# Kernel tuning notes

Measured on AMD Instinct MI355X. Metric: run time of the kernel, lower is better.

## Reference

```python
import jax, jax.numpy as jnp
import numpy as np

C = 4          # num_components
B = 2          # true batch
HEADS = 24
DIM_HEAD = 64
D = HEADS * DIM_HEAD      # 1536, attn.out_dim == query dim
CROSS = 2048              # encoder hidden dim
S = 2048                  # latent sequence length
E = 77                    # encoder sequence length
PAD = 77                  # pad_length (must equal E for the broadcast in the original code)


def setup_inputs() -> dict:
    key = jax.random.key(0)
    ks = jax.random.split(key, 12)
    w = 0.02
    return {
        "hidden_states": jax.random.normal(ks[0], (B * C, S, D), jnp.float32),
        "encoder_hidden_states": jax.random.normal(ks[1], (B * C, E, CROSS), jnp.float32),
        "Wq": jax.random.normal(ks[2], (D, D), jnp.float32) * w,
        "bq": jax.random.normal(ks[3], (D,), jnp.float32) * w,
        "Wk": jax.random.normal(ks[4], (D, CROSS), jnp.float32) * w,
        "bk": jax.random.normal(ks[5], (D,), jnp.float32) * w,
        "Wv": jax.random.normal(ks[6], (D, CROSS), jnp.float32) * w,
        "bv": jax.random.normal(ks[7], (D,), jnp.float32) * w,
        "Wo": jax.random.normal(ks[8], (D, D), jnp.float32) * w,
        "bo": jax.random.normal(ks[9], (D,), jnp.float32) * w,
        "pad_length": PAD,
    }


def reference(hidden_states, encoder_hidden_states, Wq, bq, Wk, bk, Wv, bv, Wo, bo, pad_length):
    BC, S_, D_ = hidden_states.shape
    E_ = encoder_hidden_states.shape[1]
    Bsz = BC // C
    scale = 1.0 / np.sqrt(DIM_HEAD)

    # projections (torch nn.Linear: x @ W.T + b)
    q = hidden_states @ Wq.T + bq                      # [BC, S, D]
    k = encoder_hidden_states @ Wk.T + bk              # [BC, E, D]
    v = encoder_hidden_states @ Wv.T + bv              # [BC, E, D]
    # pad branch: to_k/to_v applied to zeros -> just the bias, broadcast over pad tokens
    k_pad = jnp.broadcast_to(bk, (BC, pad_length, D_))  # [BC, PAD, D]
    v_pad = jnp.broadcast_to(bv, (BC, pad_length, D_))
    v = jnp.concatenate([v, v_pad], axis=1)            # [BC, E+PAD, D]

    # split heads
    qh = q.reshape(BC, S_, HEADS, DIM_HEAD)
    kh = k.reshape(BC, E_, HEADS, DIM_HEAD)
    kph = k_pad.reshape(BC, pad_length, HEADS, DIM_HEAD)
    vh = v.reshape(BC, E_ + pad_length, HEADS, DIM_HEAD)

    # scores: [BC, H, S, E] and [BC, H, S, PAD]
    scores = jnp.einsum("bihd,bjhd->bhij", qh, kh) * scale
    scores_pad = jnp.einsum("bihd,bjhd->bhij", qh, kph) * scale

    # component-wise softmax: view as [C, B, H, S, *], softmax over component axis 0
    scores = scores.reshape(C, Bsz, HEADS, S_, E_)
    scores_pad = scores_pad.reshape(C, Bsz, HEADS, S_, pad_length)
    w_main = jax.nn.softmax(scores, axis=0)
    w_pad = jax.nn.softmax(scores_pad, axis=0) * (C / pad_length) * (1.0 - w_main)

    w_main = w_main.reshape(BC, HEADS, S_, E_)
    w_pad = w_pad.reshape(BC, HEADS, S_, pad_length)
    weights = jnp.concatenate([w_main, w_pad], axis=-1)  # [BC, H, S, E+PAD]

    # attention @ V -> merge heads
    out = jnp.einsum("bhij,bjhd->bihd", weights, vh).reshape(BC, S_, D_)
    out = out @ Wo.T + bo   # to_out[0]; dropout is identity in eval
    return out
```

## Files before the change

kernel.cpp:

```cpp
#include <hip/hip_runtime.h>
#include <hip/hip_bf16.h>


typedef __attribute__((ext_vector_type(8))) short short8;
typedef __attribute__((ext_vector_type(4))) float f32x4;
typedef __attribute__((ext_vector_type(4))) _Float16 half4;

#define DEV __device__ __forceinline__

DEV ushort f2bf(float x) {
  __hip_bfloat16 h = __float2bfloat16(x);
  return *reinterpret_cast<ushort*>(&h);
}


__global__ __launch_bounds__(256) void cvt_f32_bf16(const float* __restrict__ in,
                                                    ushort* __restrict__ out, int n4) {
  int idx = blockIdx.x * blockDim.x + threadIdx.x;
  int stride = gridDim.x * blockDim.x;
  for (int q = idx; q < n4; q += stride) {
    float4 f = reinterpret_cast<const float4*>(in)[q];
    ushort4 o;
    o.x = f2bf(f.x); o.y = f2bf(f.y); o.z = f2bf(f.z); o.w = f2bf(f.w);
    reinterpret_cast<ushort4*>(out)[q] = o;
  }
}

__global__ __launch_bounds__(256) void cvt_w4(const float* __restrict__ w0, ushort* __restrict__ o0, int m0,
                                              const float* __restrict__ w1, ushort* __restrict__ o1, int m1,
                                              const float* __restrict__ w2, ushort* __restrict__ o2, int m2,
                                              const float* __restrict__ w3, ushort* __restrict__ o3, int m3) {
  const float* in; ushort* out; int n4;
  switch (blockIdx.y) {
    case 0: in = w0; out = o0; n4 = m0; break;
    case 1: in = w1; out = o1; n4 = m1; break;
    case 2: in = w2; out = o2; n4 = m2; break;
    default: in = w3; out = o3; n4 = m3; break;
  }
  int idx = blockIdx.x * blockDim.x + threadIdx.x;
  int stride = gridDim.x * blockDim.x;
  for (int q = idx; q < n4; q += stride) {
    float4 f = reinterpret_cast<const float4*>(in)[q];
    ushort4 o;
    o.x = f2bf(f.x); o.y = f2bf(f.y); o.z = f2bf(f.z); o.w = f2bf(f.w);
    reinterpret_cast<ushort4*>(out)[q] = o;
  }
}

__global__ __launch_bounds__(256) void cvt_pad_ehs(const float* __restrict__ in,
                                                   ushort* __restrict__ out) {
  int q = blockIdx.x * blockDim.x + threadIdx.x;
  if (q >= 640 * 2048 / 4) return;
  int r = (q * 4) >> 11;
  ushort4 o;
  if (r < 616) {
    float4 f = reinterpret_cast<const float4*>(in)[q];
    o.x = f2bf(f.x); o.y = f2bf(f.y); o.z = f2bf(f.z); o.w = f2bf(f.w);
  } else {
    o.x = 0; o.y = 0; o.z = 0; o.w = 0;
  }
  reinterpret_cast<ushort4*>(out)[q] = o;
}


template <typename OutT>
DEV void gemm_body(const ushort* __restrict__ A, const ushort* __restrict__ B,
                   const float* __restrict__ bias, OutT* __restrict__ C,
                   int M, int N, int K) {
  __shared__ __align__(16) ushort lds[32768];
  const int tid = threadIdx.x;
  const int lane = tid & 63;
  const int wid = tid >> 6;
  const int wr = wid >> 1, wc = wid & 1;
  const long m0 = (long)blockIdx.x * 128;
  const long n0 = (long)blockIdx.y * 128;
  const int ll = lane & 15, g = lane >> 4;
  const int swz = ll & 7;

  const int srow = wid * 8 + (lane >> 3);
  const int scol = ((lane & 7) ^ (lane >> 3)) * 8;
  const ushort* pa = A + (m0 + srow) * (long)K + scol;
  const ushort* pb = B + (n0 + srow) * (long)K + scol;
  const long qstep = 32 * (long)K;

  f32x4 acc[4][4] = {};

#define STAGE(tt, bsel)                                                                    \
  do {                                                                                     \
    const long kt_ = (long)(tt) * 64;                                                      \
    const int ab_ = (bsel) * 32768 + wid * 1024;                                           \
    _Pragma("unroll") for (int q = 0; q < 4; ++q)                                          \
        __builtin_amdgcn_global_load_lds(                                                  \
            (const __attribute__((address_space(1))) void*)(pa + kt_ + q * qstep),         \
            (__attribute__((address_space(3))) void*)((char*)lds + ab_ + q * 4096),        \
            16, 0, 0);                                                                     \
    _Pragma("unroll") for (int q = 0; q < 4; ++q)                                          \
        __builtin_amdgcn_global_load_lds(                                                  \
            (const __attribute__((address_space(1))) void*)(pb + kt_ + q * qstep),         \
            (__attribute__((address_space(3))) void*)((char*)lds + ab_ + 16384 + q * 4096),\
            16, 0, 0);                                                                     \
  } while (0)

  const int nt = K >> 6;
  STAGE(0, 0);
  STAGE(1, 1);
  asm volatile("s_waitcnt vmcnt(8)" ::: "memory");
  __builtin_amdgcn_s_barrier();

  for (int t = 0; t < nt; ++t) {
    const int buf = t & 1;
    const char* abase = (const char*)lds + buf * 32768;
    const char* bbase = abase + 16384;
    short8 af[4][2], bfr[4][2];
#pragma unroll
    for (int m = 0; m < 4; ++m)
#pragma unroll
      for (int ks = 0; ks < 2; ++ks)
        af[m][ks] = *reinterpret_cast<const short8*>(
            abase + (wr * 64 + m * 16 + ll) * 128 + (((ks * 4 + g) ^ swz) * 16));
#pragma unroll
    for (int n = 0; n < 4; ++n)
#pragma unroll
      for (int ks = 0; ks < 2; ++ks)
        bfr[n][ks] = *reinterpret_cast<const short8*>(
            bbase + (wc * 64 + n * 16 + ll) * 128 + (((ks * 4 + g) ^ swz) * 16));
    asm volatile("s_waitcnt lgkmcnt(0)" ::: "memory");
    __builtin_amdgcn_s_barrier();

    if (t < nt - 2) {
      STAGE(t + 2, buf);
      asm volatile("s_waitcnt vmcnt(8)" ::: "memory");
    } else if (t == nt - 2) {
      asm volatile("s_waitcnt vmcnt(0)" ::: "memory");
    }
    __builtin_amdgcn_sched_barrier(0);
    __builtin_amdgcn_s_setprio(1);
#pragma unroll
    for (int ks = 0; ks < 2; ++ks)
#pragma unroll
      for (int m = 0; m < 4; ++m)
#pragma unroll
        for (int n = 0; n < 4; ++n)
          acc[m][n] =
              __builtin_amdgcn_mfma_f32_16x16x32_bf16(af[m][ks], bfr[n][ks], acc[m][n], 0, 0, 0);
    __builtin_amdgcn_s_setprio(0);
    __builtin_amdgcn_s_barrier();
  }
#undef STAGE

#pragma unroll
  for (int m = 0; m < 4; ++m) {
#pragma unroll
    for (int n = 0; n < 4; ++n) {
      const int row = wr * 64 + m * 16 + g * 4;
      const int col = wc * 64 + n * 16 + ll;
      const float bias_v = bias[n0 + col];
#pragma unroll
      for (int r = 0; r < 4; ++r) {
        float val = acc[m][n][r] + bias_v;
        long off = (m0 + row + r) * (long)N + n0 + col;
        if constexpr (sizeof(OutT) == 2) {
          C[off] = (OutT)f2bf(val);
        } else {
          C[off] = val;
        }
      }
    }
  }
}

template <typename OutT>
__global__ __launch_bounds__(256) void gemm_p(const ushort* __restrict__ A,
                                              const ushort* __restrict__ B,
                                              const float* __restrict__ bias,
                                              OutT* __restrict__ C, int M, int N, int K) {
  gemm_body<OutT>(A, B, bias, C, M, N, K);
}

__global__ __launch_bounds__(256) void gemm_p_kv(const ushort* __restrict__ A,
                                                 const ushort* __restrict__ Bk,
                                                 const float* __restrict__ bk, float* Ck,
                                                 const ushort* __restrict__ Bv,
                                                 const float* __restrict__ bv, float* Cv,
                                                 int M, int N, int K) {
  if (blockIdx.z == 0)
    gemm_body<float>(A, Bk, bk, Ck, M, N, K);
  else
    gemm_body<float>(A, Bv, bv, Cv, M, N, K);
}


__global__ __launch_bounds__(256) void prep_kv(const float* __restrict__ k_f,
                                               const float* __restrict__ v_f,
                                               const float* __restrict__ bk,
                                               const float* __restrict__ bv,
                                               ushort* __restrict__ kimg,
                                               ushort* __restrict__ vimg) {
  __shared__ _Float16 vl[80][68];
  const int c = blockIdx.x, h = blockIdx.y, bb = blockIdx.z;
  const int tid = threadIdx.x;
  const long ibase = ((long)(bb * 24 + h)) * 20480 + c * 5120;

  for (int rr = tid; rr < 640; rr += 256) {
    int j = rr >> 3, t = rr & 7;
    short8 v = {};
    const float* src = nullptr;
    if (j < 77)
      src = k_f + ((long)((c * 2 + bb) * 77 + j)) * 1536 + h * 64 + t * 8;
    else if (j == 77)
      src = bk + h * 64 + t * 8;
    if (src) {
      float4 f0 = reinterpret_cast<const float4*>(src)[0];
      float4 f1 = reinterpret_cast<const float4*>(src)[1];
      v[0] = f2bf(f0.x); v[1] = f2bf(f0.y); v[2] = f2bf(f0.z); v[3] = f2bf(f0.w);
      v[4] = f2bf(f1.x); v[5] = f2bf(f1.y); v[6] = f2bf(f1.z); v[7] = f2bf(f1.w);
    }
    *reinterpret_cast<short8*>(kimg + ibase + j * 64 + (t ^ (j & 7)) * 8) = v;
  }
  for (int rr = tid; rr < 640; rr += 256) {
    int j = rr >> 3, t = rr & 7;
    half4 lo = {}, hi = {};
    const float* src = nullptr;
    if (j < 77)
      src = v_f + ((long)((c * 2 + bb) * 77 + j)) * 1536 + h * 64 + t * 8;
    else if (j == 77)
      src = bv + h * 64 + t * 8;
    if (src) {
      float4 f0 = reinterpret_cast<const float4*>(src)[0];
      float4 f1 = reinterpret_cast<const float4*>(src)[1];
      lo[0] = (_Float16)f0.x; lo[1] = (_Float16)f0.y; lo[2] = (_Float16)f0.z; lo[3] = (_Float16)f0.w;
      hi[0] = (_Float16)f1.x; hi[1] = (_Float16)f1.y; hi[2] = (_Float16)f1.z; hi[3] = (_Float16)f1.w;
    }
    *reinterpret_cast<half4*>(&vl[j][t * 8]) = lo;
    *reinterpret_cast<half4*>(&vl[j][t * 8 + 4]) = hi;
  }
  __syncthreads();
  const int d = tid & 63, jg = tid >> 6;
  ushort* vrow = vimg + ibase + d * 80;
  const int x = (d >> 2) & 3;
#pragma unroll
  for (int b = 0; b < 5; ++b) {
    int jb = jg * 5 + b;
    half4 hv;
#pragma unroll
    for (int e = 0; e < 4; ++e) hv[e] = vl[jb * 4 + e][d];
    *reinterpret_cast<half4*>(vrow + ((jb ^ x) << 2)) = hv;
  }
}


__global__ __launch_bounds__(256) void attn_v3(const ushort* __restrict__ qg,
                                               const ushort* __restrict__ kimg,
                                               const ushort* __restrict__ vimg,
                                               ushort* __restrict__ ao) {
  __shared__ __align__(16) ushort kl[20480];
  __shared__ __align__(16) ushort vt[20480];
  const int tid = threadIdx.x;
  const int lane = tid & 63;
  const int w = tid >> 6;
  const int h = blockIdx.y, bb = blockIdx.z;
  const int i0 = blockIdx.x * 64;
  const long ib = ((long)(bb * 24 + h)) * 20480;

#pragma unroll
  for (int p = 0; p < 10; ++p) {
    int is = p * 4 + w;
    __builtin_amdgcn_global_load_lds(
        (const __attribute__((address_space(1))) void*)(kimg + ib + is * 512 + lane * 8),
        (__attribute__((address_space(3))) void*)((char*)kl + is * 1024), 16, 0, 0);
    __builtin_amdgcn_global_load_lds(
        (const __attribute__((address_space(1))) void*)(vimg + ib + is * 512 + lane * 8),
        (__attribute__((address_space(3))) void*)((char*)vt + is * 1024), 16, 0, 0);
  }
  __syncthreads();

  const int ll = lane & 15, g = lane >> 4;

  f32x4 s[4][5];
#pragma unroll
  for (int c = 0; c < 4; ++c)
#pragma unroll
    for (int m = 0; m < 5; ++m) s[c][m] = (f32x4){0.f, 0.f, 0.f, 0.f};

#pragma unroll
  for (int c = 0; c < 4; ++c) {
    const ushort* qbase =
        qg + ((long)((c * 2 + bb) * 2048 + i0 + w * 16 + ll)) * 1536 + h * 64 + g * 8;
    short8 qf0 = *reinterpret_cast<const short8*>(qbase);
    short8 qf1 = *reinterpret_cast<const short8*>(qbase + 32);
#pragma unroll
    for (int m = 0; m < 5; ++m) {
      const char* base = (const char*)kl + c * 10240 + (m * 16 + ll) * 128;
      short8 a0 = *reinterpret_cast<const short8*>(base + ((g ^ (ll & 7)) * 16));
      short8 a1 = *reinterpret_cast<const short8*>(base + (((4 + g) ^ (ll & 7)) * 16));
      s[c][m] = __builtin_amdgcn_mfma_f32_16x16x32_bf16(a0, qf0, s[c][m], 0, 0, 0);
      s[c][m] = __builtin_amdgcn_mfma_f32_16x16x32_bf16(a1, qf1, s[c][m], 0, 0, 0);
    }
  }

  const float scale = 0.125f;
  float wsum0 = 0.f, wsum1 = 0.f, wsum2 = 0.f, wsum3 = 0.f;
#pragma unroll
  for (int m = 0; m < 5; ++m) {
#pragma unroll
    for (int e = 0; e < 4; ++e) {
      float x0 = s[0][m][e] * scale, x1 = s[1][m][e] * scale;
      float x2 = s[2][m][e] * scale, x3 = s[3][m][e] * scale;
      float mx = fmaxf(fmaxf(x0, x1), fmaxf(x2, x3));
      float e0 = __expf(x0 - mx), e1 = __expf(x1 - mx);
      float e2 = __expf(x2 - mx), e3 = __expf(x3 - mx);
      float inv = __fdividef(1.f, e0 + e1 + e2 + e3);
      float w0 = e0 * inv, w1 = e1 * inv, w2 = e2 * inv, w3 = e3 * inv;
      int jj = m * 16 + g * 4 + e;
      float msk = (jj < 77) ? 1.f : 0.f;
      wsum0 += w0 * msk; wsum1 += w1 * msk; wsum2 += w2 * msk; wsum3 += w3 * msk;
      s[0][m][e] = w0; s[1][m][e] = w1; s[2][m][e] = w2; s[3][m][e] = w3;
    }
  }
  wsum0 += __shfl_xor(wsum0, 16); wsum0 += __shfl_xor(wsum0, 32);
  wsum1 += __shfl_xor(wsum1, 16); wsum1 += __shfl_xor(wsum1, 32);
  wsum2 += __shfl_xor(wsum2, 16); wsum2 += __shfl_xor(wsum2, 32);
  wsum3 += __shfl_xor(wsum3, 16); wsum3 += __shfl_xor(wsum3, 32);

  const bool g3 = (g == 3);
  {
    float wsum[4] = {wsum0, wsum1, wsum2, wsum3};
#pragma unroll
    for (int c = 0; c < 4; ++c) {
      float w77 = s[c][4][1];
      float pwv = w77 * (4.0f / 77.0f) * (77.0f - wsum[c]);
      s[c][4][1] = g3 ? pwv : w77;
      s[c][4][2] = g3 ? 0.f : s[c][4][2];
      s[c][4][3] = g3 ? 0.f : s[c][4][3];
    }
  }

  half4 wf[4][5];
#pragma unroll
  for (int c = 0; c < 4; ++c)
#pragma unroll
    for (int m = 0; m < 5; ++m) {
      half4 hv;
      hv[0] = (_Float16)s[c][m][0];
      hv[1] = (_Float16)s[c][m][1];
      hv[2] = (_Float16)s[c][m][2];
      hv[3] = (_Float16)s[c][m][3];
      wf[c][m] = hv;
    }

  f32x4 o[4][4];
#pragma unroll
  for (int c = 0; c < 4; ++c)
#pragma unroll
    for (int n = 0; n < 4; ++n) o[c][n] = (f32x4){0.f, 0.f, 0.f, 0.f};

#pragma unroll
  for (int c = 0; c < 4; ++c)
#pragma unroll
    for (int m = 0; m < 5; ++m)
#pragma unroll
      for (int n = 0; n < 4; ++n) {
        const int dd = n * 16 + ll;
        const int jb = (m * 4 + g) ^ ((dd >> 2) & 3);
        half4 vf = *reinterpret_cast<const half4*>(
            reinterpret_cast<const _Float16*>(vt) + c * 5120 + dd * 80 + (jb << 2));
        o[c][n] = __builtin_amdgcn_mfma_f32_16x16x16f16(wf[c][m], vf, o[c][n], 0, 0, 0);
      }

#pragma unroll
  for (int c = 0; c < 4; ++c)
#pragma unroll
    for (int n = 0; n < 4; ++n)
#pragma unroll
      for (int r = 0; r < 4; ++r) {
        long row = (long)((c * 2 + bb) * 2048 + i0 + w * 16 + g * 4 + r);
        ao[row * 1536 + h * 64 + n * 16 + ll] = f2bf(o[c][n][r]);
      }
}


extern "C" void kernel_launch(void* const* d_in, const int* in_sizes, int n_in,
                              void* d_out, int out_size, void* d_ws, size_t ws_size,
                              hipStream_t stream) {
  (void)in_sizes; (void)n_in; (void)out_size; (void)ws_size;
  const float* hs  = (const float*)d_in[0];
  const float* ehs = (const float*)d_in[1];
  const float* Wq  = (const float*)d_in[2];
  const float* bq  = (const float*)d_in[3];
  const float* Wk  = (const float*)d_in[4];
  const float* bk  = (const float*)d_in[5];
  const float* Wv  = (const float*)d_in[6];
  const float* bv  = (const float*)d_in[7];
  const float* Wo  = (const float*)d_in[8];
  const float* bo  = (const float*)d_in[9];
  float* out = (float*)d_out;

  char* ws = (char*)d_ws;
  size_t off = 0;
  auto alloc = [&](size_t bytes) {
    char* p = ws + off;
    off += (bytes + 255) & ~(size_t)255;
    return p;
  };
  ushort* hs_bf  = (ushort*)alloc(16384UL * 1536 * 2);
  ushort* ehs_bf = (ushort*)alloc(640UL * 2048 * 2);
  ushort* Wq_bf  = (ushort*)alloc(1536UL * 1536 * 2);
  ushort* Wk_bf  = (ushort*)alloc(1536UL * 2048 * 2);
  ushort* Wv_bf  = (ushort*)alloc(1536UL * 2048 * 2);
  ushort* Wo_bf  = (ushort*)alloc(1536UL * 1536 * 2);
  ushort* q_bf   = (ushort*)alloc(16384UL * 1536 * 2);
  float*  k_f    = (float*)alloc(640UL * 1536 * 4);
  float*  v_f    = (float*)alloc(640UL * 1536 * 4);
  ushort* ao_bf  = (ushort*)alloc(16384UL * 1536 * 2);
  ushort* kimg   = (ushort*)alloc(48UL * 20480 * 2);
  ushort* vimg   = (ushort*)alloc(48UL * 20480 * 2);

  dim3 b256(256);
  cvt_f32_bf16<<<2048, b256, 0, stream>>>(hs, hs_bf, 16384 * 1536 / 4);
  cvt_pad_ehs<<<(640 * 2048 / 4 + 255) / 256, b256, 0, stream>>>(ehs, ehs_bf);
  cvt_w4<<<dim3(768, 4), b256, 0, stream>>>(Wq, Wq_bf, 1536 * 1536 / 4,
                                            Wk, Wk_bf, 1536 * 2048 / 4,
                                            Wv, Wv_bf, 1536 * 2048 / 4,
                                            Wo, Wo_bf, 1536 * 1536 / 4);

  gemm_p_kv<<<dim3(5, 12, 2), b256, 0, stream>>>(ehs_bf, Wk_bf, bk, k_f, Wv_bf, bv, v_f,
                                                 640, 1536, 2048);
  prep_kv<<<dim3(4, 24, 2), b256, 0, stream>>>(k_f, v_f, bk, bv, kimg, vimg);
  gemm_p<ushort><<<dim3(128, 12), b256, 0, stream>>>(hs_bf, Wq_bf, bq, q_bf, 16384, 1536, 1536);
  attn_v3<<<dim3(32, 24, 2), b256, 0, stream>>>(q_bf, kimg, vimg, ao_bf);
  gemm_p<float><<<dim3(128, 12), b256, 0, stream>>>(ao_bf, Wo_bf, bo, out, 16384, 1536, 1536);
}
```

Before: 270.4 us.

## Replace Q/O projection GEMMs with 256x256-tile double-buffered direct-to-LDS kernel

Adds a new GEMM kernel with 256x256 output tiles, 512 threads, 128KB of dynamic LDS double-buffered through global_load_lds, XCD-aware block swizzling and split MFMA phases with priority hints. It is used for the large Q and output projections in place of the 128x128 kernel, to raise data reuse per tile and overlap loads with compute. It also merges the three fp32-to-bf16 conversion launches into a single kernel. The large LDS footprint and register pressure limit occupancy, and the 384-block grid may leave some CUs with an uneven share of work.

```diff
diff --git a/kernel.cpp b/kernel.cpp
--- a/kernel.cpp
+++ b/kernel.cpp
@@ -14,52 +14,43 @@
 }
 
 
-__global__ __launch_bounds__(256) void cvt_f32_bf16(const float* __restrict__ in,
-                                                    ushort* __restrict__ out, int n4) {
+__global__ __launch_bounds__(256) void cvt_all(const float* __restrict__ hs, ushort* __restrict__ hs_bf,
+                                               const float* __restrict__ Wq, ushort* __restrict__ Wq_bf,
+                                               const float* __restrict__ Wk, ushort* __restrict__ Wk_bf,
+                                               const float* __restrict__ Wv, ushort* __restrict__ Wv_bf,
+                                               const float* __restrict__ Wo, ushort* __restrict__ Wo_bf,
+                                               const float* __restrict__ ehs, ushort* __restrict__ ehs_bf) {
+  const int b0 = 6291456;
+  const int b1 = b0 + 589824;
+  const int b2 = b1 + 786432;
+  const int b3 = b2 + 786432;
+  const int b4 = b3 + 589824;
+  const int total = b4 + 327680;
   int idx = blockIdx.x * blockDim.x + threadIdx.x;
   int stride = gridDim.x * blockDim.x;
-  for (int q = idx; q < n4; q += stride) {
-    float4 f = reinterpret_cast<const float4*>(in)[q];
+  for (int q = idx; q < total; q += stride) {
+    const float* in; ushort* out; int qq;
+    bool zero = false;
+    if (q < b0)      { in = hs;  out = hs_bf;  qq = q; }
+    else if (q < b1) { in = Wq;  out = Wq_bf;  qq = q - b0; }
+    else if (q < b2) { in = Wk;  out = Wk_bf;  qq = q - b1; }
+    else if (q < b3) { in = Wv;  out = Wv_bf;  qq = q - b2; }
+    else if (q < b4) { in = Wo;  out = Wo_bf;  qq = q - b3; }
+    else {
+      qq = q - b4;
+      int r = qq >> 9;
+      in = ehs; out = ehs_bf;
+      zero = (r >= 616);
+    }
     ushort4 o;
-    o.x = f2bf(f.x); o.y = f2bf(f.y); o.z = f2bf(f.z); o.w = f2bf(f.w);
-    reinterpret_cast<ushort4*>(out)[q] = o;
-  }
-}
-
-__global__ __launch_bounds__(256) void cvt_w4(const float* __restrict__ w0, ushort* __restrict__ o0, int m0,
-                                              const float* __restrict__ w1, ushort* __restrict__ o1, int m1,
-                                              const float* __restrict__ w2, ushort* __restrict__ o2, int m2,
-                                              const float* __restrict__ w3, ushort* __restrict__ o3, int m3) {
-  const float* in; ushort* out; int n4;
-  switch (blockIdx.y) {
-    case 0: in = w0; out = o0; n4 = m0; break;
-    case 1: in = w1; out = o1; n4 = m1; break;
-    case 2: in = w2; out = o2; n4 = m2; break;
-    default: in = w3; out = o3; n4 = m3; break;
-  }
-  int idx = blockIdx.x * blockDim.x + threadIdx.x;
-  int stride = gridDim.x * blockDim.x;
-  for (int q = idx; q < n4; q += stride) {
-    float4 f = reinterpret_cast<const float4*>(in)[q];
-    ushort4 o;
-    o.x = f2bf(f.x); o.y = f2bf(f.y); o.z = f2bf(f.z); o.w = f2bf(f.w);
-    reinterpret_cast<ushort4*>(out)[q] = o;
-  }
-}
-
-__global__ __launch_bounds__(256) void cvt_pad_ehs(const float* __restrict__ in,
-                                                   ushort* __restrict__ out) {
-  int q = blockIdx.x * blockDim.x + threadIdx.x;
-  if (q >= 640 * 2048 / 4) return;
-  int r = (q * 4) >> 11;
-  ushort4 o;
-  if (r < 616) {
-    float4 f = reinterpret_cast<const float4*>(in)[q];
-    o.x = f2bf(f.x); o.y = f2bf(f.y); o.z = f2bf(f.z); o.w = f2bf(f.w);
-  } else {
-    o.x = 0; o.y = 0; o.z = 0; o.w = 0;
-  }
-  reinterpret_cast<ushort4*>(out)[q] = o;
+    if (!zero) {
+      float4 f = reinterpret_cast<const float4*>(in)[qq];
+      o.x = f2bf(f.x); o.y = f2bf(f.y); o.z = f2bf(f.z); o.w = f2bf(f.w);
+    } else {
+      o.x = 0; o.y = 0; o.z = 0; o.w = 0;
+    }
+    reinterpret_cast<ushort4*>(out)[qq] = o;
+  }
 }
 
 
@@ -169,14 +160,6 @@
   }
 }
 
-template <typename OutT>
-__global__ __launch_bounds__(256) void gemm_p(const ushort* __restrict__ A,
-                                              const ushort* __restrict__ B,
-                                              const float* __restrict__ bias,
-                                              OutT* __restrict__ C, int M, int N, int K) {
-  gemm_body<OutT>(A, B, bias, C, M, N, K);
-}
-
 __global__ __launch_bounds__(256) void gemm_p_kv(const ushort* __restrict__ A,
                                                  const ushort* __restrict__ Bk,
                                                  const float* __restrict__ bk, float* Ck,
@@ -187,6 +170,139 @@
     gemm_body<float>(A, Bk, bk, Ck, M, N, K);
   else
     gemm_body<float>(A, Bv, bv, Cv, M, N, K);
+}
+
+
+template <typename OutT>
+__global__ __launch_bounds__(512, 2) void gemm256(const ushort* __restrict__ A,
+                                                  const ushort* __restrict__ B,
+                                                  const float* __restrict__ bias,
+                                                  OutT* __restrict__ C,
+                                                  int M, int N, int K, int nnx) {
+  extern __shared__ char dynlds[];
+  const int tid = threadIdx.x;
+  const int lane = tid & 63;
+  const int w = tid >> 6;
+  const int wr = w >> 2, wc = w & 3;
+  const int ll = lane & 15, g = lane >> 4;
+  const int swz = ll & 7;
+
+  const int cpx = gridDim.x >> 3;
+  const int sw = (blockIdx.x & 7) * cpx + (blockIdx.x >> 3);
+  const long m0 = (long)(sw / nnx) * 256;
+  const long n0 = (long)(sw % nnx) * 256;
+
+  const int srow = tid >> 3;
+  const int scol = ((tid & 7) ^ ((tid >> 3) & 7)) * 8;
+  const ushort* pa = A + (m0 + srow) * (long)K + scol;
+  const ushort* pb = B + (n0 + srow) * (long)K + scol;
+  const long rstep = 64 * (long)K;
+
+  f32x4 acc[8][4] = {};
+
+#define STAGE2(tt, bsel)                                                                    \
+  do {                                                                                      \
+    const long kt_ = (long)(tt) * 64;                                                       \
+    char* ab_ = dynlds + (bsel) * 65536;                                                    \
+    _Pragma("unroll") for (int q = 0; q < 4; ++q)                                           \
+        __builtin_amdgcn_global_load_lds(                                                   \
+            (const __attribute__((address_space(1))) void*)(pa + kt_ + q * rstep),          \
+            (__attribute__((address_space(3))) void*)(ab_ + q * 8192 + tid * 16),           \
+            16, 0, 0);                                                                      \
+    _Pragma("unroll") for (int q = 0; q < 4; ++q)                                           \
+        __builtin_amdgcn_global_load_lds(                                                   \
+            (const __attribute__((address_space(1))) void*)(pb + kt_ + q * rstep),          \
+            (__attribute__((address_space(3))) void*)(ab_ + 32768 + q * 8192 + tid * 16),   \
+            16, 0, 0);                                                                      \
+  } while (0)
+
+  const int nt = K >> 6;
+  STAGE2(0, 0);
+  STAGE2(1, 1);
+  asm volatile("s_waitcnt vmcnt(8)" ::: "memory");
+  __builtin_amdgcn_s_barrier();
+  __builtin_amdgcn_sched_barrier(0);
+
+  for (int t = 0; t < nt; ++t) {
+    const int buf = t & 1;
+    const char* abase = dynlds + buf * 65536;
+    const char* bbase = abase + 32768;
+    short8 alo[4][2], bfr[4][2], ahi[4][2];
+#pragma unroll
+    for (int m = 0; m < 4; ++m)
+#pragma unroll
+      for (int ks = 0; ks < 2; ++ks)
+        alo[m][ks] = *reinterpret_cast<const short8*>(
+            abase + (wr * 128 + m * 16 + ll) * 128 + (((ks * 4 + g) ^ swz) * 16));
+#pragma unroll
+    for (int n = 0; n < 4; ++n)
+#pragma unroll
+      for (int ks = 0; ks < 2; ++ks)
+        bfr[n][ks] = *reinterpret_cast<const short8*>(
+            bbase + (wc * 64 + n * 16 + ll) * 128 + (((ks * 4 + g) ^ swz) * 16));
+    asm volatile("s_waitcnt lgkmcnt(0)" ::: "memory");
+    __builtin_amdgcn_sched_barrier(0);
+    __builtin_amdgcn_s_setprio(1);
+#pragma unroll
+    for (int ks = 0; ks < 2; ++ks)
+#pragma unroll
+      for (int m = 0; m < 4; ++m)
+#pragma unroll
+        for (int n = 0; n < 4; ++n)
+          acc[m][n] =
+              __builtin_amdgcn_mfma_f32_16x16x32_bf16(alo[m][ks], bfr[n][ks], acc[m][n], 0, 0, 0);
+    __builtin_amdgcn_s_setprio(0);
+#pragma unroll
+    for (int m = 0; m < 4; ++m)
+#pragma unroll
+      for (int ks = 0; ks < 2; ++ks)
+        ahi[m][ks] = *reinterpret_cast<const short8*>(
+            abase + (wr * 128 + 64 + m * 16 + ll) * 128 + (((ks * 4 + g) ^ swz) * 16));
+    asm volatile("s_waitcnt lgkmcnt(0)" ::: "memory");
+    __builtin_amdgcn_sched_barrier(0);
+    __builtin_amdgcn_s_barrier();
+
+    if (t < nt - 2) {
+      STAGE2(t + 2, buf);
+      asm volatile("s_waitcnt vmcnt(8)" ::: "memory");
+    } else if (t == nt - 2) {
+      asm volatile("s_waitcnt vmcnt(0)" ::: "memory");
+    }
+    __builtin_amdgcn_sched_barrier(0);
+    __builtin_amdgcn_s_setprio(1);
+#pragma unroll
+    for (int ks = 0; ks < 2; ++ks)
+#pragma unroll
+      for (int m = 0; m < 4; ++m)
+#pragma unroll
+        for (int n = 0; n < 4; ++n)
+          acc[4 + m][n] =
+              __builtin_amdgcn_mfma_f32_16x16x32_bf16(ahi[m][ks], bfr[n][ks], acc[4 + m][n], 0, 0, 0);
+    __builtin_amdgcn_s_setprio(0);
+    __builtin_amdgcn_s_barrier();
+    __builtin_amdgcn_sched_barrier(0);
+  }
+#undef STAGE2
+
+#pragma unroll
+  for (int m = 0; m < 8; ++m) {
+#pragma unroll
+    for (int n = 0; n < 4; ++n) {
+      const int row = wr * 128 + m * 16 + g * 4;
+      const int col = wc * 64 + n * 16 + ll;
+      const float bias_v = bias[n0 + col];
+#pragma unroll
+      for (int r = 0; r < 4; ++r) {
+        float val = acc[m][n][r] + bias_v;
+        long off = (m0 + row + r) * (long)N + n0 + col;
+        if constexpr (sizeof(OutT) == 2) {
+          C[off] = (OutT)f2bf(val);
+        } else {
+          C[off] = val;
+        }
+      }
+    }
+  }
 }
 
 
@@ -415,18 +531,19 @@
   ushort* kimg   = (ushort*)alloc(48UL * 20480 * 2);
   ushort* vimg   = (ushort*)alloc(48UL * 20480 * 2);
 
+  hipFuncSetAttribute(reinterpret_cast<const void*>(&gemm256<ushort>),
+                      hipFuncAttributeMaxDynamicSharedMemorySize, 131072);
+  hipFuncSetAttribute(reinterpret_cast<const void*>(&gemm256<float>),
+                      hipFuncAttributeMaxDynamicSharedMemorySize, 131072);
+
   dim3 b256(256);
-  cvt_f32_bf16<<<2048, b256, 0, stream>>>(hs, hs_bf, 16384 * 1536 / 4);
-  cvt_pad_ehs<<<(640 * 2048 / 4 + 255) / 256, b256, 0, stream>>>(ehs, ehs_bf);
-  cvt_w4<<<dim3(768, 4), b256, 0, stream>>>(Wq, Wq_bf, 1536 * 1536 / 4,
-                                            Wk, Wk_bf, 1536 * 2048 / 4,
-                                            Wv, Wv_bf, 1536 * 2048 / 4,
-                                            Wo, Wo_bf, 1536 * 1536 / 4);
+  cvt_all<<<4096, b256, 0, stream>>>(hs, hs_bf, Wq, Wq_bf, Wk, Wk_bf, Wv, Wv_bf,
+                                     Wo, Wo_bf, ehs, ehs_bf);
 
   gemm_p_kv<<<dim3(5, 12, 2), b256, 0, stream>>>(ehs_bf, Wk_bf, bk, k_f, Wv_bf, bv, v_f,
                                                  640, 1536, 2048);
   prep_kv<<<dim3(4, 24, 2), b256, 0, stream>>>(k_f, v_f, bk, bv, kimg, vimg);
-  gemm_p<ushort><<<dim3(128, 12), b256, 0, stream>>>(hs_bf, Wq_bf, bq, q_bf, 16384, 1536, 1536);
+  gemm256<ushort><<<384, 512, 131072, stream>>>(hs_bf, Wq_bf, bq, q_bf, 16384, 1536, 1536, 6);
   attn_v3<<<dim3(32, 24, 2), b256, 0, stream>>>(q_bf, kimg, vimg, ao_bf);
-  gemm_p<float><<<dim3(128, 12), b256, 0, stream>>>(ao_bf, Wo_bf, bo, out, 16384, 1536, 1536);
-}
+  gemm256<float><<<384, 512, 131072, stream>>>(ao_bf, Wo_bf, bo, out, 16384, 1536, 1536, 6);
+}
```

After: 288.4 us. 6.7% more time.

## Merge conversion kernels and read K fragments directly from global memory

Applied to the files above, without the earlier changes.

Folds the three f32-to-bf16 conversion kernels into a single grid-stride kernel, removing two launches. In the attention kernel, K is no longer staged in LDS: each wave loads its MFMA K fragments straight from the pre-swizzled global image. The V LDS load is issued up front and its barrier moved after the softmax, so the V copy overlaps the QK and softmax work. This halves LDS use per block, which may raise occupancy, at the cost of redundant global or L2 reads of K across the four waves.

```diff
diff --git a/kernel.cpp b/kernel.cpp
--- a/kernel.cpp
+++ b/kernel.cpp
@@ -14,52 +14,43 @@
 }
 
 
-__global__ __launch_bounds__(256) void cvt_f32_bf16(const float* __restrict__ in,
-                                                    ushort* __restrict__ out, int n4) {
+__global__ __launch_bounds__(256) void cvt_all(const float* __restrict__ hs, ushort* __restrict__ hs_bf,
+                                               const float* __restrict__ Wq, ushort* __restrict__ Wq_bf,
+                                               const float* __restrict__ Wk, ushort* __restrict__ Wk_bf,
+                                               const float* __restrict__ Wv, ushort* __restrict__ Wv_bf,
+                                               const float* __restrict__ Wo, ushort* __restrict__ Wo_bf,
+                                               const float* __restrict__ ehs, ushort* __restrict__ ehs_bf) {
+  const int b0 = 6291456;
+  const int b1 = b0 + 589824;
+  const int b2 = b1 + 786432;
+  const int b3 = b2 + 786432;
+  const int b4 = b3 + 589824;
+  const int total = b4 + 327680;
   int idx = blockIdx.x * blockDim.x + threadIdx.x;
   int stride = gridDim.x * blockDim.x;
-  for (int q = idx; q < n4; q += stride) {
-    float4 f = reinterpret_cast<const float4*>(in)[q];
+  for (int q = idx; q < total; q += stride) {
+    const float* in; ushort* out; int qq;
+    bool zero = false;
+    if (q < b0)      { in = hs;  out = hs_bf;  qq = q; }
+    else if (q < b1) { in = Wq;  out = Wq_bf;  qq = q - b0; }
+    else if (q < b2) { in = Wk;  out = Wk_bf;  qq = q - b1; }
+    else if (q < b3) { in = Wv;  out = Wv_bf;  qq = q - b2; }
+    else if (q < b4) { in = Wo;  out = Wo_bf;  qq = q - b3; }
+    else {
+      qq = q - b4;
+      int r = qq >> 9;
+      in = ehs; out = ehs_bf;
+      zero = (r >= 616);
+    }
     ushort4 o;
-    o.x = f2bf(f.x); o.y = f2bf(f.y); o.z = f2bf(f.z); o.w = f2bf(f.w);
-    reinterpret_cast<ushort4*>(out)[q] = o;
-  }
-}
-
-__global__ __launch_bounds__(256) void cvt_w4(const float* __restrict__ w0, ushort* __restrict__ o0, int m0,
-                                              const float* __restrict__ w1, ushort* __restrict__ o1, int m1,
-                                              const float* __restrict__ w2, ushort* __restrict__ o2, int m2,
-                                              const float* __restrict__ w3, ushort* __restrict__ o3, int m3) {
-  const float* in; ushort* out; int n4;
-  switch (blockIdx.y) {
-    case 0: in = w0; out = o0; n4 = m0; break;
-    case 1: in = w1; out = o1; n4 = m1; break;
-    case 2: in = w2; out = o2; n4 = m2; break;
-    default: in = w3; out = o3; n4 = m3; break;
-  }
-  int idx = blockIdx.x * blockDim.x + threadIdx.x;
-  int stride = gridDim.x * blockDim.x;
-  for (int q = idx; q < n4; q += stride) {
-    float4 f = reinterpret_cast<const float4*>(in)[q];
-    ushort4 o;
-    o.x = f2bf(f.x); o.y = f2bf(f.y); o.z = f2bf(f.z); o.w = f2bf(f.w);
-    reinterpret_cast<ushort4*>(out)[q] = o;
-  }
-}
-
-__global__ __launch_bounds__(256) void cvt_pad_ehs(const float* __restrict__ in,
-                                                   ushort* __restrict__ out) {
-  int q = blockIdx.x * blockDim.x + threadIdx.x;
-  if (q >= 640 * 2048 / 4) return;
-  int r = (q * 4) >> 11;
-  ushort4 o;
-  if (r < 616) {
-    float4 f = reinterpret_cast<const float4*>(in)[q];
-    o.x = f2bf(f.x); o.y = f2bf(f.y); o.z = f2bf(f.z); o.w = f2bf(f.w);
-  } else {
-    o.x = 0; o.y = 0; o.z = 0; o.w = 0;
-  }
-  reinterpret_cast<ushort4*>(out)[q] = o;
+    if (!zero) {
+      float4 f = reinterpret_cast<const float4*>(in)[qq];
+      o.x = f2bf(f.x); o.y = f2bf(f.y); o.z = f2bf(f.z); o.w = f2bf(f.w);
+    } else {
+      o.x = 0; o.y = 0; o.z = 0; o.w = 0;
+    }
+    reinterpret_cast<ushort4*>(out)[qq] = o;
+  }
 }
 
 
@@ -249,11 +240,10 @@
 }
 
 
-__global__ __launch_bounds__(256) void attn_v3(const ushort* __restrict__ qg,
+__global__ __launch_bounds__(256) void attn_v4(const ushort* __restrict__ qg,
                                                const ushort* __restrict__ kimg,
                                                const ushort* __restrict__ vimg,
                                                ushort* __restrict__ ao) {
-  __shared__ __align__(16) ushort kl[20480];
   __shared__ __align__(16) ushort vt[20480];
   const int tid = threadIdx.x;
   const int lane = tid & 63;
@@ -266,13 +256,9 @@
   for (int p = 0; p < 10; ++p) {
     int is = p * 4 + w;
     __builtin_amdgcn_global_load_lds(
-        (const __attribute__((address_space(1))) void*)(kimg + ib + is * 512 + lane * 8),
-        (__attribute__((address_space(3))) void*)((char*)kl + is * 1024), 16, 0, 0);
-    __builtin_amdgcn_global_load_lds(
         (const __attribute__((address_space(1))) void*)(vimg + ib + is * 512 + lane * 8),
         (__attribute__((address_space(3))) void*)((char*)vt + is * 1024), 16, 0, 0);
   }
-  __syncthreads();
 
   const int ll = lane & 15, g = lane >> 4;
 
@@ -288,11 +274,12 @@
         qg + ((long)((c * 2 + bb) * 2048 + i0 + w * 16 + ll)) * 1536 + h * 64 + g * 8;
     short8 qf0 = *reinterpret_cast<const short8*>(qbase);
     short8 qf1 = *reinterpret_cast<const short8*>(qbase + 32);
+    const ushort* kbase = kimg + ib + c * 5120;
 #pragma unroll
     for (int m = 0; m < 5; ++m) {
-      const char* base = (const char*)kl + c * 10240 + (m * 16 + ll) * 128;
-      short8 a0 = *reinterpret_cast<const short8*>(base + ((g ^ (ll & 7)) * 16));
-      short8 a1 = *reinterpret_cast<const short8*>(base + (((4 + g) ^ (ll & 7)) * 16));
+      const ushort* rb = kbase + (m * 16 + ll) * 64;
+      short8 a0 = *reinterpret_cast<const short8*>(rb + (g ^ (ll & 7)) * 8);
+      short8 a1 = *reinterpret_cast<const short8*>(rb + ((4 + g) ^ (ll & 7)) * 8);
       s[c][m] = __builtin_amdgcn_mfma_f32_16x16x32_bf16(a0, qf0, s[c][m], 0, 0, 0);
       s[c][m] = __builtin_amdgcn_mfma_f32_16x16x32_bf16(a1, qf1, s[c][m], 0, 0, 0);
     }
@@ -347,6 +334,8 @@
       hv[3] = (_Float16)s[c][m][3];
       wf[c][m] = hv;
     }
+
+  __syncthreads();
 
   f32x4 o[4][4];
 #pragma unroll
@@ -416,17 +405,13 @@
   ushort* vimg   = (ushort*)alloc(48UL * 20480 * 2);
 
   dim3 b256(256);
-  cvt_f32_bf16<<<2048, b256, 0, stream>>>(hs, hs_bf, 16384 * 1536 / 4);
-  cvt_pad_ehs<<<(640 * 2048 / 4 + 255) / 256, b256, 0, stream>>>(ehs, ehs_bf);
-  cvt_w4<<<dim3(768, 4), b256, 0, stream>>>(Wq, Wq_bf, 1536 * 1536 / 4,
-                                            Wk, Wk_bf, 1536 * 2048 / 4,
-                                            Wv, Wv_bf, 1536 * 2048 / 4,
-                                            Wo, Wo_bf, 1536 * 1536 / 4);
+  cvt_all<<<4096, b256, 0, stream>>>(hs, hs_bf, Wq, Wq_bf, Wk, Wk_bf, Wv, Wv_bf,
+                                     Wo, Wo_bf, ehs, ehs_bf);
 
   gemm_p_kv<<<dim3(5, 12, 2), b256, 0, stream>>>(ehs_bf, Wk_bf, bk, k_f, Wv_bf, bv, v_f,
                                                  640, 1536, 2048);
   prep_kv<<<dim3(4, 24, 2), b256, 0, stream>>>(k_f, v_f, bk, bv, kimg, vimg);
   gemm_p<ushort><<<dim3(128, 12), b256, 0, stream>>>(hs_bf, Wq_bf, bq, q_bf, 16384, 1536, 1536);
-  attn_v3<<<dim3(32, 24, 2), b256, 0, stream>>>(q_bf, kimg, vimg, ao_bf);
+  attn_v4<<<dim3(32, 24, 2), b256, 0, stream>>>(q_bf, kimg, vimg, ao_bf);
   gemm_p<float><<<dim3(128, 12), b256, 0, stream>>>(ao_bf, Wo_bf, bo, out, 16384, 1536, 1536);
 }
```

Measured after the change: 268.2 us, median of 2. Within noise of the previous version (-0.8%).
